# Optimization experiments

Measured on AMD Instinct MI355X. Metric: run time of the kernel, lower is better.

The kernel has to match this reference:

```python
import jax, jax.numpy as jnp
import numpy as np
from jax import lax


def setup_inputs() -> dict:
    key = jax.random.key(0)
    ks = jax.random.split(key, 6)
    B, L, Cin, N, Cout = 4, 4096, 256, 512, 256
    s = 0.02
    return {
        "x": jax.random.normal(ks[0], (B, L, Cin), dtype=jnp.float32),
        "Wx": jax.random.normal(ks[1], (Cin, N), dtype=jnp.float32) * s,
        "bx": jnp.zeros((N,), dtype=jnp.float32),
        "Wbc": jax.random.normal(ks[2], (Cin, 2 * N), dtype=jnp.float32) * s,
        "bbc": jnp.zeros((2 * N,), dtype=jnp.float32),
        "Wd": jax.random.normal(ks[3], (Cin, N), dtype=jnp.float32) * s,
        "bd": jnp.zeros((N,), dtype=jnp.float32),
        "Wy": jax.random.normal(ks[4], (N, Cout), dtype=jnp.float32) * s,
        "by": jnp.zeros((Cout,), dtype=jnp.float32),
    }


def _scan_combine(c1, c2):
    # linear recurrence h_t = a_t * h_{t-1} + b_t as an associative op
    a1, b1 = c1
    a2, b2 = c2
    return a1 * a2, a2 * b1 + b2


def reference(x, Wx, bx, Wbc, bbc, Wd, bd, Wy, by):
    # projections: [B, L, N]
    x_proj = x @ Wx + bx
    BC = x @ Wbc + bbc
    delta = x @ Wd + bd
    Bm, C = jnp.split(BC, 2, axis=-1)

    A_bar = jnp.exp(-jax.nn.softplus(delta))      # [B, L, N], in (0, 1)
    B_bar = (1.0 - A_bar) * Bm                    # [B, L, N]

    # selective scan (h0 = 0): h_t = A_bar_t * h_{t-1} + B_bar_t * x_proj_t
    u = B_bar * x_proj
    _, h = lax.associative_scan(_scan_combine, (A_bar, u), axis=1)

    y = C * h                                      # [B, L, N]
    return y @ Wy + by                             # [B, L, Cout]
```

## Files before the change

kernel.cpp:

```cpp
#include <hip/hip_runtime.h>
#include <hip/hip_fp16.h>
#include <math.h>

constexpr int CIN  = 256;
constexpr int NST  = 512;
constexpr int LSEQ = 4096;
constexpr int BB   = 4;
constexpr int ROWS = BB * LSEQ;
constexpr int COUT = 256;
constexpr int LC   = 32;
constexpr int NC   = LSEQ / LC;

typedef __attribute__((ext_vector_type(8))) short bf16x8;
typedef __attribute__((ext_vector_type(4))) float f32x4;
typedef unsigned short ushort_t;
typedef unsigned int   uint_t;

__device__ __forceinline__ ushort_t f2bf(float f) {
    uint_t u = __float_as_uint(f);
    u = (u + 0x7FFF + ((u >> 16) & 1)) >> 16;
    return (ushort_t)u;
}
__device__ __forceinline__ float bf2f(ushort_t s) {
    return __uint_as_float(((uint_t)s) << 16);
}

constexpr int WELEMS  = 4 * NST * CIN + COUT * NST;
constexpr int WBLOCKS = WELEMS / 256;
constexpr int XBLOCKS = (ROWS * CIN / 4) / 256;

__global__ __launch_bounds__(256)
void prep_kernel(const float* __restrict__ Wx, const float* __restrict__ Wbc,
                 const float* __restrict__ Wd, const float* __restrict__ Wy,
                 const float* __restrict__ x,
                 ushort_t* __restrict__ Wt, ushort_t* __restrict__ Wyt,
                 ushort_t* __restrict__ xb)
{
    const int bid = blockIdx.x;
    if (bid < WBLOCKS) {
        const int gid = bid * 256 + threadIdx.x;
        if (gid < 4 * NST * CIN) {
            const int mat = gid >> 17;
            const int idx = gid & 131071;
            const int k   = idx >> 9;
            const int n   = idx & 511;
            float v;
            if      (mat == 0) v = Wx [k * NST + n];
            else if (mat == 1) v = Wbc[k * (2 * NST) + n];
            else if (mat == 2) v = Wbc[k * (2 * NST) + NST + n];
            else               v = Wd [k * NST + n];
            Wt[((size_t)mat * NST + n) * CIN + k] = f2bf(v);
        } else {
            const int idx = gid - 4 * NST * CIN;
            const int k   = idx >> 8;
            const int n   = idx & 255;
            Wyt[(size_t)n * NST + k] = f2bf(Wy[k * COUT + n]);
        }
    } else {
        const int i = ((bid - WBLOCKS) * 256 + threadIdx.x) * 4;
        float4 v = *(const float4*)&x[i];
        uint2 o;
        o.x = (uint_t)f2bf(v.x) | ((uint_t)f2bf(v.y) << 16);
        o.y = (uint_t)f2bf(v.z) | ((uint_t)f2bf(v.w) << 16);
        *(uint2*)&xb[i] = o;
    }
}

__global__ __launch_bounds__(256, 3)
void proj_mfma_kernel(const ushort_t* __restrict__ xb, const ushort_t* __restrict__ Wt,
                      const float* __restrict__ bx, const float* __restrict__ bbc,
                      const float* __restrict__ bd,
                      uint_t* __restrict__ AU, ushort_t* __restrict__ CYb,
                      float2* __restrict__ AHc)
{
    __shared__ alignas(16) char smem[46080];
    ushort_t (*xs)[72]     = (ushort_t(*)[72])smem;
    ushort_t (*ws)[64][72] = (ushort_t(*)[64][72])(smem + 9216);
    float2   (*aus)[65]    = (float2(*)[65])smem;
    float2   (*comb)[64]   = (float2(*)[64])(smem + 33280);
    ushort_t (*cs)[72]     = (ushort_t(*)[72])(smem + 35328);

    const int tid  = threadIdx.x;
    const int wave = tid >> 6;
    const int lane = tid & 63;
    const int lm   = lane & 15;
    const int lq   = lane >> 4;
    const int row0 = blockIdx.x * 64;
    const int n0   = blockIdx.y * 64;

    const int sr = tid >> 2;
    const int sk = (tid & 3) << 4;

    f32x4 acc[4][4];
    #pragma unroll
    for (int rt = 0; rt < 4; ++rt)
        #pragma unroll
        for (int m = 0; m < 4; ++m)
            acc[rt][m] = (f32x4){0.f, 0.f, 0.f, 0.f};

    const ushort_t* xsrc  = xb + (size_t)(row0 + sr) * CIN + sk;
    const ushort_t* wsrc0 = Wt + (size_t)(n0 + sr) * CIN + sk;

    for (int k0 = 0; k0 < CIN; k0 += 64) {
        uint4 xv0 = *(const uint4*)(xsrc + k0);
        uint4 xv1 = *(const uint4*)(xsrc + k0 + 8);
        uint4 wv[4][2];
        #pragma unroll
        for (int m = 0; m < 4; ++m) {
            const ushort_t* p = wsrc0 + (size_t)m * NST * CIN + k0;
            wv[m][0] = *(const uint4*)(p);
            wv[m][1] = *(const uint4*)(p + 8);
        }
        *(uint4*)&xs[sr][sk]     = xv0;
        *(uint4*)&xs[sr][sk + 8] = xv1;
        #pragma unroll
        for (int m = 0; m < 4; ++m) {
            *(uint4*)&ws[m][sr][sk]     = wv[m][0];
            *(uint4*)&ws[m][sr][sk + 8] = wv[m][1];
        }
        __syncthreads();

        #pragma unroll
        for (int ks = 0; ks < 2; ++ks) {
            const int kk = ks * 32 + lq * 8;
            bf16x8 af[4], bf[4];
            #pragma unroll
            for (int rt = 0; rt < 4; ++rt)
                af[rt] = *(const bf16x8*)&xs[rt * 16 + lm][kk];
            #pragma unroll
            for (int m = 0; m < 4; ++m)
                bf[m] = *(const bf16x8*)&ws[m][wave * 16 + lm][kk];
            #pragma unroll
            for (int rt = 0; rt < 4; ++rt)
                #pragma unroll
                for (int m = 0; m < 4; ++m)
                    acc[rt][m] = __builtin_amdgcn_mfma_f32_16x16x32_bf16(
                        af[rt], bf[m], acc[rt][m], 0, 0, 0);
        }
        __syncthreads();
    }

    const int nl = wave * 16 + lm;
    const int ng = n0 + nl;
    const float bxv = bx [ng];
    const float bbv = bbc[ng];
    const float bcv = bbc[NST + ng];
    const float bdv = bd [ng];
    #pragma unroll
    for (int rt = 0; rt < 4; ++rt) {
        #pragma unroll
        for (int r = 0; r < 4; ++r) {
            const int t   = rt * 16 + lq * 4 + r;
            const int row = row0 + t;
            float xp = acc[rt][0][r] + bxv;
            float bm = acc[rt][1][r] + bbv;
            float cc = acc[rt][2][r] + bcv;
            float dd = acc[rt][3][r] + bdv;
            dd = fminf(dd, 60.0f);
            float e  = __expf(dd);
            float A  = 1.0f / (1.0f + e);
            float u  = (e * A) * bm * xp;
            const size_t idx = (size_t)row * NST + ng;
            __half2 hv = __floats2half2_rn(A, u);
            __builtin_nontemporal_store(__builtin_bit_cast(uint_t, hv), &AU[idx]);
            aus[t][nl] = make_float2(A, u);
            cs[t][nl]  = f2bf(cc);
        }
    }
    __syncthreads();

    {
        const int r  = tid >> 2;
        const int ns = (tid & 3) << 4;
        uint4 c0 = *(const uint4*)&cs[r][ns];
        uint4 c1 = *(const uint4*)&cs[r][ns + 8];
        ushort_t* dst = CYb + (size_t)(row0 + r) * NST + n0 + ns;
        *(uint4*)dst       = c0;
        *(uint4*)(dst + 8) = c1;
    }

    {
        const int n  = tid & 63;
        const int sg = tid >> 6;
        float ap = 1.0f, h = 0.0f;
        #pragma unroll
        for (int i = 0; i < 16; ++i) {
            float2 au = aus[sg * 16 + i][n];
            ap *= au.x;
            h  = fmaf(au.x, h, au.y);
        }
        comb[sg][n] = make_float2(ap, h);
    }
    __syncthreads();

    if (tid < 128) {
        const int n  = tid & 63;
        const int ch = tid >> 6;
        float2 c0 = comb[ch * 2 + 0][n];
        float2 c1 = comb[ch * 2 + 1][n];
        const size_t ci = (size_t)(blockIdx.x * 2 + ch) * NST + (n0 + n);
        AHc[ci] = make_float2(c0.x * c1.x, fmaf(c1.x, c0.y, c1.y));
    }
}

__global__ __launch_bounds__(256)
void scan_carry_kernel(const float2* __restrict__ AHc, float* __restrict__ Carry2)
{
    const int wid  = (blockIdx.x * 256 + threadIdx.x) >> 6;
    const int lane = threadIdx.x & 63;
    const int b = wid >> 9;
    const int n = wid & (NST - 1);

    float2 v0 = AHc[(size_t)(b * NC + lane) * NST + n];
    float a = v0.x, h = v0.y;
    #pragma unroll
    for (int d = 1; d < 64; d <<= 1) {
        float ao = __shfl_up(a, d, 64);
        float ho = __shfl_up(h, d, 64);
        if (lane >= d) { h = fmaf(a, ho, h); a *= ao; }
    }
    float c0 = __shfl_up(h, 1, 64);
    if (lane == 0) c0 = 0.0f;
    const float Ht = __shfl(h, 63, 64);

    float2 v1 = AHc[(size_t)(b * NC + 64 + lane) * NST + n];
    float a1 = v1.x, h1 = v1.y;
    #pragma unroll
    for (int d = 1; d < 64; d <<= 1) {
        float ao = __shfl_up(a1, d, 64);
        float ho = __shfl_up(h1, d, 64);
        if (lane >= d) { h1 = fmaf(a1, ho, h1); a1 *= ao; }
    }
    float pa = __shfl_up(a1, 1, 64);
    float ph = __shfl_up(h1, 1, 64);
    if (lane == 0) { pa = 1.0f; ph = 0.0f; }
    float c1 = fmaf(pa, Ht, ph);

    float* cp = Carry2 + (size_t)(b * NST + n) * NC;
    cp[lane]      = c0;
    cp[64 + lane] = c1;
}

__global__ __launch_bounds__(256)
void scan_final_kernel(const uint_t* __restrict__ AU, ushort_t* __restrict__ CYb,
                       const float* __restrict__ Carry2)
{
    const int gid = blockIdx.x * 256 + threadIdx.x;
    const int n   = gid & (NST - 1);
    const int bc  = gid >> 9;
    const int b   = bc >> 7;
    const int c   = bc & (NC - 1);
    const size_t base = (size_t)bc * LC * NST + n;
    float h = Carry2[((size_t)b * NST + n) * NC + c];
    #pragma unroll 8
    for (int t = 0; t < LC; ++t) {
        size_t idx = base + (size_t)t * NST;
        uint_t raw = __builtin_nontemporal_load(&AU[idx]);
        float2 au  = __half22float2(__builtin_bit_cast(__half2, raw));
        float cc   = bf2f(CYb[idx]);
        h = fmaf(au.x, h, au.y);
        CYb[idx] = f2bf(cc * h);
    }
}

__global__ __launch_bounds__(256, 4)
void out_mfma_kernel(const ushort_t* __restrict__ yb, const ushort_t* __restrict__ Wyt,
                     const float* __restrict__ by, float* __restrict__ out)
{
    __shared__ alignas(16) ushort_t ys [64][72];
    __shared__ alignas(16) ushort_t wys[64][72];

    const int tid  = threadIdx.x;
    const int wave = tid >> 6;
    const int lane = tid & 63;
    const int lm   = lane & 15;
    const int lq   = lane >> 4;
    const int row0 = blockIdx.x * 64;
    const int n0   = blockIdx.y * 64;

    const int sr = tid >> 2;
    const int sk = (tid & 3) << 4;

    f32x4 acc[4];
    #pragma unroll
    for (int rt = 0; rt < 4; ++rt) acc[rt] = (f32x4){0.f, 0.f, 0.f, 0.f};

    const ushort_t* ysrc = yb  + (size_t)(row0 + sr) * NST + sk;
    const ushort_t* wsrc = Wyt + (size_t)(n0  + sr) * NST + sk;

    for (int k0 = 0; k0 < NST; k0 += 64) {
        uint4 yv0 = *(const uint4*)(ysrc + k0);
        uint4 yv1 = *(const uint4*)(ysrc + k0 + 8);
        uint4 wv0 = *(const uint4*)(wsrc + k0);
        uint4 wv1 = *(const uint4*)(wsrc + k0 + 8);
        *(uint4*)&ys [sr][sk]     = yv0;
        *(uint4*)&ys [sr][sk + 8] = yv1;
        *(uint4*)&wys[sr][sk]     = wv0;
        *(uint4*)&wys[sr][sk + 8] = wv1;
        __syncthreads();

        #pragma unroll
        for (int ks = 0; ks < 2; ++ks) {
            const int kk = ks * 32 + lq * 8;
            bf16x8 bfr = *(const bf16x8*)&wys[wave * 16 + lm][kk];
            #pragma unroll
            for (int rt = 0; rt < 4; ++rt) {
                bf16x8 af = *(const bf16x8*)&ys[rt * 16 + lm][kk];
                acc[rt] = __builtin_amdgcn_mfma_f32_16x16x32_bf16(
                    af, bfr, acc[rt], 0, 0, 0);
            }
        }
        __syncthreads();
    }

    const int ng = n0 + wave * 16 + lm;
    const float bv = by[ng];
    #pragma unroll
    for (int rt = 0; rt < 4; ++rt)
        #pragma unroll
        for (int r = 0; r < 4; ++r) {
            const int row = row0 + rt * 16 + lq * 4 + r;
            out[(size_t)row * COUT + ng] = acc[rt][r] + bv;
        }
}

extern "C" void kernel_launch(void* const* d_in, const int* in_sizes, int n_in,
                              void* d_out, int out_size, void* d_ws, size_t ws_size,
                              hipStream_t stream)
{
    const float* x   = (const float*)d_in[0];
    const float* Wx  = (const float*)d_in[1];
    const float* bx  = (const float*)d_in[2];
    const float* Wbc = (const float*)d_in[3];
    const float* bbc = (const float*)d_in[4];
    const float* Wd  = (const float*)d_in[5];
    const float* bd  = (const float*)d_in[6];
    const float* Wy  = (const float*)d_in[7];
    const float* by  = (const float*)d_in[8];
    float* out = (float*)d_out;

    char* p = (char*)d_ws;
    uint_t*   AU     = (uint_t*)p;        p += (size_t)ROWS * NST * 4;
    ushort_t* CYb    = (ushort_t*)p;      p += (size_t)ROWS * NST * 2;
    ushort_t* xb     = (ushort_t*)p;      p += (size_t)ROWS * CIN * 2;
    ushort_t* Wt     = (ushort_t*)p;      p += (size_t)4 * NST * CIN * 2;
    ushort_t* Wyt    = (ushort_t*)p;      p += (size_t)COUT * NST * 2;
    float2*   AHc    = (float2*)p;        p += (size_t)BB * NC * NST * 8;
    float*    Carry2 = (float*)p;         p += (size_t)BB * NST * NC * 4;

    prep_kernel<<<WBLOCKS + XBLOCKS, 256, 0, stream>>>(
        Wx, Wbc, Wd, Wy, x, Wt, Wyt, xb);

    proj_mfma_kernel<<<dim3(ROWS / 64, NST / 64), 256, 0, stream>>>(
        xb, Wt, bx, bbc, bd, AU, CYb, AHc);

    scan_carry_kernel<<<(BB * NST) / 4, 256, 0, stream>>>(AHc, Carry2);

    scan_final_kernel<<<(BB * NC * NST) / 256, 256, 0, stream>>>(
        AU, CYb, Carry2);

    out_mfma_kernel<<<dim3(ROWS / 64, COUT / 64), 256, 0, stream>>>(
        CYb, Wyt, by, out);
}
```

Before: 147.8 us.

## Register-prefetch next K tile in projection GEMM; use cached AU loads/stores

The projection GEMM now loads the next 64-wide K slice of x and weights into registers right after the barrier, so those global loads overlap the MFMA work on the current tile instead of stalling at the top of each iteration. Separately, the nontemporal store and load of the packed A/u buffer become ordinary accesses, so the data can stay in L2/MALL between the projection kernel and the final scan kernel. The prefetch raises register pressure in a kernel with 64 accumulator floats, which may lower occupancy. Dropping the nontemporal hints may also evict other data from cache.

```diff
diff --git a/kernel.cpp b/kernel.cpp
--- a/kernel.cpp
+++ b/kernel.cpp
@@ -101,24 +101,36 @@
     const ushort_t* xsrc  = xb + (size_t)(row0 + sr) * CIN + sk;
     const ushort_t* wsrc0 = Wt + (size_t)(n0 + sr) * CIN + sk;
 
+    uint4 xv0 = *(const uint4*)(xsrc);
+    uint4 xv1 = *(const uint4*)(xsrc + 8);
+    uint4 wv0[4], wv1[4];
+    #pragma unroll
+    for (int m = 0; m < 4; ++m) {
+        const ushort_t* p = wsrc0 + (size_t)m * NST * CIN;
+        wv0[m] = *(const uint4*)(p);
+        wv1[m] = *(const uint4*)(p + 8);
+    }
+
     for (int k0 = 0; k0 < CIN; k0 += 64) {
-        uint4 xv0 = *(const uint4*)(xsrc + k0);
-        uint4 xv1 = *(const uint4*)(xsrc + k0 + 8);
-        uint4 wv[4][2];
-        #pragma unroll
-        for (int m = 0; m < 4; ++m) {
-            const ushort_t* p = wsrc0 + (size_t)m * NST * CIN + k0;
-            wv[m][0] = *(const uint4*)(p);
-            wv[m][1] = *(const uint4*)(p + 8);
-        }
         *(uint4*)&xs[sr][sk]     = xv0;
         *(uint4*)&xs[sr][sk + 8] = xv1;
         #pragma unroll
         for (int m = 0; m < 4; ++m) {
-            *(uint4*)&ws[m][sr][sk]     = wv[m][0];
-            *(uint4*)&ws[m][sr][sk + 8] = wv[m][1];
+            *(uint4*)&ws[m][sr][sk]     = wv0[m];
+            *(uint4*)&ws[m][sr][sk + 8] = wv1[m];
         }
         __syncthreads();
+
+        if (k0 + 64 < CIN) {
+            xv0 = *(const uint4*)(xsrc + k0 + 64);
+            xv1 = *(const uint4*)(xsrc + k0 + 72);
+            #pragma unroll
+            for (int m = 0; m < 4; ++m) {
+                const ushort_t* p = wsrc0 + (size_t)m * NST * CIN + k0 + 64;
+                wv0[m] = *(const uint4*)(p);
+                wv1[m] = *(const uint4*)(p + 8);
+            }
+        }
 
         #pragma unroll
         for (int ks = 0; ks < 2; ++ks) {
@@ -162,7 +174,7 @@
             float u  = (e * A) * bm * xp;
             const size_t idx = (size_t)row * NST + ng;
             __half2 hv = __floats2half2_rn(A, u);
-            __builtin_nontemporal_store(__builtin_bit_cast(uint_t, hv), &AU[idx]);
+            AU[idx] = __builtin_bit_cast(uint_t, hv);
             aus[t][nl] = make_float2(A, u);
             cs[t][nl]  = f2bf(cc);
         }
@@ -255,7 +267,7 @@
     #pragma unroll 8
     for (int t = 0; t < LC; ++t) {
         size_t idx = base + (size_t)t * NST;
-        uint_t raw = __builtin_nontemporal_load(&AU[idx]);
+        uint_t raw = AU[idx];
         float2 au  = __half22float2(__builtin_bit_cast(__half2, raw));
         float cc   = bf2f(CYb[idx]);
         h = fmaf(au.x, h, au.y);
```

After: 193.0 us. +30.6%, slower.
